# Kernel optimization log

Hardware: AMD Instinct MI355X
Metric: run time of the kernel (lower is better)

The kernel has to match this reference:

```python
import jax, jax.numpy as jnp
import numpy as np

TRAN_DIM = 768
N_HEADS = 8
HEAD_DIM = 96
INNER = N_HEADS * HEAD_DIM  # 768


def setup_inputs() -> dict:
    key = jax.random.key(0)
    k1, k2, k3, k4, k5 = jax.random.split(key, 5)
    x = jax.random.normal(k1, (16, 1024, TRAN_DIM), dtype=jnp.float32)
    s_in = 1.0 / np.sqrt(TRAN_DIM)
    W_qkv = jax.random.uniform(k2, (TRAN_DIM, INNER * 3), jnp.float32, -s_in, s_in)
    b_qkv = jax.random.uniform(k3, (INNER * 3,), jnp.float32, -s_in, s_in)
    s_o = 1.0 / np.sqrt(INNER)
    W_out = jax.random.uniform(k4, (INNER, TRAN_DIM), jnp.float32, -s_o, s_o)
    b_out = jax.random.uniform(k5, (TRAN_DIM,), jnp.float32, -s_o, s_o)
    return {"x": x, "W_qkv": W_qkv, "b_qkv": b_qkv, "W_out": W_out, "b_out": b_out}


def reference(x, W_qkv, b_qkv, W_out, b_out):
    B, N, _ = x.shape
    qkv = x @ W_qkv + b_qkv  # [B, N, 3*INNER]
    q, k, v = jnp.split(qkv, 3, axis=-1)
    # [B, N, INNER] -> [B, H, N, D]
    def to_heads(t):
        return t.reshape(B, N, N_HEADS, HEAD_DIM).transpose(0, 2, 1, 3)
    q, k, v = to_heads(q), to_heads(k), to_heads(v)
    scale = HEAD_DIM ** (-0.5)
    dots = jnp.einsum('bhnd,bhmd->bhnm', q, k) * scale
    attn = jax.nn.softmax(dots, axis=-1)
    out = jnp.einsum('bhnm,bhmd->bhnd', attn, v)
    out = out.transpose(0, 2, 1, 3).reshape(B, N, INNER)
    return out @ W_out + b_out
```

## Files before the change

### kernel.cpp

```cpp
#include <hip/hip_runtime.h>
#include <hip/hip_bf16.h>


#define DEVINL __device__ __forceinline__

typedef __attribute__((ext_vector_type(8))) short s16x8;
typedef __attribute__((ext_vector_type(4))) short s16x4;
typedef __attribute__((ext_vector_type(4))) float f32x4;
typedef __attribute__((ext_vector_type(16))) float f32x16;

DEVINL short f2bf(float f) {
  union { float f; unsigned u; } c; c.f = f;
  unsigned r = c.u + 0x7FFFu + ((c.u >> 16) & 1u);
  return (short)(r >> 16);
}
DEVINL float asf(unsigned u) {
  union { unsigned u; float f; } c; c.u = u; return c.f;
}
DEVINL unsigned pack2(float a, float b) {
  union { float f; unsigned u; } ca, cb; ca.f = a; cb.f = b;
  return (ca.u >> 16) | (cb.u & 0xffff0000u);
}
DEVINL int swap23(int k) { return (k & ~12) | ((k & 4) << 1) | ((k & 8) >> 1); }

DEVINL void gload_lds16(const short* g, short* lds) {
  __builtin_amdgcn_global_load_lds((const __attribute__((address_space(1))) void*)g,
                                   (__attribute__((address_space(3))) void*)lds, 16, 0, 0);
}


__global__ void cvt_x_kernel(const float* __restrict__ in, short* __restrict__ out) {
  int i = blockIdx.x * 256 + threadIdx.x;
  float4 v = ((const float4*)in)[i];
  s16x4 o = { f2bf(v.x), f2bf(v.y), f2bf(v.z), f2bf(v.w) };
  *(s16x4*)(out + (size_t)i * 4) = o;
}

__global__ void tcvt_kernel(const float* __restrict__ in, short* __restrict__ out, int R, int C) {
  __shared__ float t[32][33];
  int tx = threadIdx.x & 31, ty = threadIdx.x >> 5;
  int r0 = blockIdx.y * 32, c0 = blockIdx.x * 32;
#pragma unroll
  for (int i = 0; i < 4; i++) {
    int r = ty + i * 8;
    t[r][tx] = in[(size_t)(r0 + r) * C + c0 + tx];
  }
  __syncthreads();
#pragma unroll
  for (int i = 0; i < 4; i++) {
    int r = ty + i * 8;
    out[(size_t)(c0 + r) * R + r0 + tx] = f2bf(t[tx][r]);
  }
}

__global__ void vtrans_kernel(const short* __restrict__ qkvb, short* __restrict__ out) {
  __shared__ short t[32][34];
  int tx = threadIdx.x & 31, ty = threadIdx.x >> 5;
  int d0 = blockIdx.x * 32, n0 = blockIdx.y * 32;
  int pair = blockIdx.z;
  int b = pair >> 3, h = pair & 7;
#pragma unroll
  for (int i = 0; i < 4; i++) {
    int r = ty + i * 8;
    t[r][tx] = qkvb[(size_t)(b * 1024 + n0 + r) * 2304 + 1536 + h * 96 + d0 + tx];
  }
  __syncthreads();
  size_t obase = (size_t)pair * 96 * 1024;
#pragma unroll
  for (int i = 0; i < 4; i++) {
    int r = ty + i * 8;
    out[obase + (size_t)(d0 + r) * 1024 + n0 + tx] = t[tx][r];
  }
}


template <int MODE>
__global__ __launch_bounds__(512, 4) void gemm2(const short* __restrict__ A, const short* __restrict__ Bt,
                                                const float* __restrict__ bias, int K, int nTn,
                                                short* __restrict__ qkvb, float* __restrict__ outf) {
  __shared__ short lds[32768];
  short* const ldsA = lds;
  short* const ldsB = lds + 16384;
  const int tid = threadIdx.x;
  const int l = tid & 63, w = tid >> 6;
  const int lo = l & 15, hi = l >> 4;
  const int wm = w >> 1, wn = w & 1;

  int cpx = gridDim.x >> 3;
  int bid = blockIdx.x;
  int swz = (bid & 7) * cpx + (bid >> 3);
  int tm = swz / nTn, tn = swz - tm * nTn;

  const int NKT = K >> 5;

  const int Ls = tid >> 3, s7 = tid & 7;
  const int pS = (s7 >> 2) & 1;
  const int cS = (s7 & 3) ^ (Ls & 3);
  const int rho = 2 * Ls + pS;
  const int gA = ((rho >> 5) << 6) + (rho & 31);
  const short* aS0 = A + (size_t)(tm * 256 + gA) * K + cS * 8;
  const short* aS1 = aS0 + (size_t)32 * K;
  const short* bS = Bt + (size_t)(tn * 128 + rho) * K + cS * 8;
  short* const aD = ldsA + tid * 8;
  short* const bD = ldsB + tid * 8;

#define ST_A(j, q) gload_lds16(((q) ? aS1 : aS0) + (j) * 32, aD + (((j) & 1) * 2 + (q)) * 4096)
#define ST_B(j)    gload_lds16(bS + (j) * 32, bD + ((j) & 1) * 4096)

  const int LaBase = wm * 16 + (lo >> 1);
  const int LbBase = wn * 32 + (lo >> 1);
  const int pp = (lo & 1) << 2;

  f32x4 acc[4][4] = {};

#define RD_A(AF, buf, qm) do {                                                   \
    const short* base_ = ldsA + ((buf) * 2 + (qm)) * 4096;                       \
    _Pragma("unroll") for (int mi = 0; mi < 2; mi++) {                           \
      int La_ = LaBase + mi * 8;                                                 \
      AF[mi] = *(const s16x8*)(base_ + La_ * 64 + (((hi ^ (La_ & 3)) + pp) << 3)); } } while (0)
#define RD_B(BF, buf) do {                                                       \
    const short* base_ = ldsB + (buf) * 4096;                                    \
    _Pragma("unroll") for (int b = 0; b < 4; b++) {                              \
      int Lb_ = LbBase + b * 8;                                                  \
      BF[b] = *(const s16x8*)(base_ + Lb_ * 64 + (((hi ^ (Lb_ & 3)) + pp) << 3)); } } while (0)

#define MM8(a0, AF, BF) do {                                                     \
    __builtin_amdgcn_s_setprio(1);                                               \
    _Pragma("unroll") for (int mi = 0; mi < 2; mi++)                             \
      _Pragma("unroll") for (int b = 0; b < 4; b++)                              \
        acc[(a0) + mi][b] = __builtin_amdgcn_mfma_f32_16x16x32_bf16(             \
            AF[mi], BF[b], acc[(a0) + mi][b], 0, 0, 0);                          \
    __builtin_amdgcn_s_setprio(0);                                               \
    __builtin_amdgcn_sched_barrier(0); } while (0)

#define WAITV(n) asm volatile("s_waitcnt vmcnt(" #n ")" ::: "memory")
#define BARR() do { __builtin_amdgcn_sched_barrier(0); __builtin_amdgcn_s_barrier(); \
                    __builtin_amdgcn_sched_barrier(0); } while (0)

  ST_A(0, 0); ST_A(0, 1); ST_B(0);
  ST_A(1, 0); ST_B(1);
  WAITV(2);
  __builtin_amdgcn_s_barrier();

  s16x8 af[2], bf[4];
#pragma unroll 1
  for (int kt = 0; kt < NKT; kt++) {
    int buf = kt & 1;
    RD_A(af, buf, 0);
    RD_B(bf, buf);
    MM8(0, af, bf);
    if (kt + 1 < NKT) ST_A(kt + 1, 1);
    if (kt == NKT - 1) { WAITV(0); } else { WAITV(3); }
    BARR();
    RD_A(af, buf, 1);
    MM8(2, af, bf);
    if (kt + 2 < NKT) {
      ST_A(kt + 2, 0); ST_B(kt + 2);
      WAITV(3);
    } else {
      WAITV(0);
    }
    BARR();
  }
#undef ST_A
#undef ST_B
#undef RD_A
#undef RD_B
#undef MM8
#undef WAITV
#undef BARR

  if (MODE == 0) {
    const float qscale = 0.14724444757204526f;
    __syncthreads();
#pragma unroll
    for (int b = 0; b < 4; b++) {
      int colr = wn * 64 + b * 16 + lo;
      int coln = tn * 128 + colr;
      float bv = bias[coln];
      float scl = (coln < 768) ? qscale : 1.0f;
#pragma unroll
      for (int a = 0; a < 4; a++)
#pragma unroll
        for (int j = 0; j < 4; j++) {
          int rowr = wm * 64 + a * 16 + hi * 4 + j;
          lds[rowr * 128 + colr] = f2bf((acc[a][b][j] + bv) * scl);
        }
    }
    __syncthreads();
    short* dstb = qkvb + (size_t)(tm * 256) * 2304 + tn * 128;
#pragma unroll
    for (int k = 0; k < 8; k++) {
      int g = k * 512 + tid;
      int r = g >> 4, c = g & 15;
      *(s16x8*)(dstb + (size_t)r * 2304 + c * 8) = *(const s16x8*)(lds + r * 128 + c * 8);
    }
  } else {
#pragma unroll
    for (int b = 0; b < 4; b++) {
      int coln = tn * 128 + wn * 64 + b * 16 + lo;
      float bv = bias[coln];
#pragma unroll
      for (int a = 0; a < 4; a++)
#pragma unroll
        for (int j = 0; j < 4; j++) {
          int rowm = tm * 256 + wm * 64 + a * 16 + hi * 4 + j;
          outf[(size_t)rowm * 768 + coln] = acc[a][b][j] + bv;
        }
    }
  }
}


__global__ __launch_bounds__(256) void attn_kernel(const short* __restrict__ qkvb,
                                                   const short* __restrict__ vtb,
                                                   short* __restrict__ attn_out) {
  __shared__ short Klds[64 * 104];
  __shared__ short Vlds[96 * 64];
  int tid = threadIdx.x, lane = tid & 63, wid = tid >> 6;
  int q31 = lane & 31, hi2 = lane >> 5;
  int bid = blockIdx.x;
  int pair = bid & 127, qt = bid >> 7;
  int b = pair >> 3, h = pair & 7;
  const short* Vtp = vtb + (size_t)pair * 1024 * 96;
  int qrow0 = qt * 128 + wid * 32;

  s16x8 qf[6];
#pragma unroll
  for (int dc = 0; dc < 6; dc++)
    qf[dc] = *(const s16x8*)(qkvb + (size_t)(b * 1024 + qrow0 + q31) * 2304 +
                             h * 96 + dc * 16 + hi2 * 8);

  const short* sp[6];
  short* sdst[6];
  int sstep[6];
#pragma unroll
  for (int i = 0; i < 6; i++) {
    if (i < 3) {
      int c = i * 256 + tid;
      int krow = c / 12, kcc = c - krow * 12;
      int lam = swap23(krow);
      sdst[i] = Klds + lam * 104 + kcc * 8;
      sp[i] = qkvb + (size_t)(b * 1024 + krow) * 2304 + 768 + h * 96 + kcc * 8;
      sstep[i] = 64 * 2304;
    } else {
      int d = (i - 3) * 256 + tid;
      int vrow = d >> 3, vcc = d & 7;
      sdst[i] = Vlds + vrow * 64 + ((vcc ^ (vrow & 7)) << 3);
      sp[i] = Vtp + (size_t)vrow * 1024 + vcc * 8;
      sstep[i] = 64;
    }
  }

  f32x16 accO[3] = {};
  float lsum = 0.0f;

  s16x8 sreg[6];
#pragma unroll
  for (int i = 0; i < 6; i++) sreg[i] = *(const s16x8*)sp[i];

  for (int t = 0; t < 16; t++) {
    __syncthreads();
#pragma unroll
    for (int i = 0; i < 6; i++) *(s16x8*)sdst[i] = sreg[i];
    __syncthreads();

    int t2 = (t + 1) & 15;
#pragma unroll
    for (int i = 0; i < 6; i++)
      sreg[i] = *(const s16x8*)(sp[i] + (size_t)t2 * sstep[i]);

#pragma unroll
    for (int kb = 0; kb < 2; kb++) {
      f32x16 st = {};
#pragma unroll
      for (int dc = 0; dc < 6; dc++) {
        int c = dc * 2 + hi2;
        int lam = kb * 32 + q31;
        s16x8 kf = *(const s16x8*)(Klds + lam * 104 + c * 8);
        st = __builtin_amdgcn_mfma_f32_32x32x16_bf16(kf, qf[dc], st, 0, 0, 0);
      }

      unsigned u[8];
#pragma unroll
      for (int i = 0; i < 8; i++) {
        float p0 = __builtin_amdgcn_exp2f(st[2 * i]);
        float p1 = __builtin_amdgcn_exp2f(st[2 * i + 1]);
        unsigned w = pack2(p0, p1);
        u[i] = w;
        lsum += asf(w << 16) + asf(w & 0xffff0000u);
      }

#pragma unroll
      for (int half = 0; half < 2; half++) {
        union { unsigned w[4]; s16x8 v; } pa;
#pragma unroll
        for (int wi = 0; wi < 4; wi++) pa.w[wi] = u[half * 4 + wi];
        int kc = kb * 2 + half;
#pragma unroll
        for (int db = 0; db < 3; db++) {
          int d = db * 32 + q31;
          s16x8 vf = *(const s16x8*)(Vlds + d * 64 + (((kc * 2 + hi2) ^ (d & 7)) << 3));
          accO[db] = __builtin_amdgcn_mfma_f32_32x32x16_bf16(pa.v, vf, accO[db], 0, 0, 0);
        }
      }
    }
  }

  float s = lsum + __shfl_xor(lsum, 32, 64);
  float rinv = 1.0f / s;
  float rr[16];
#pragma unroll
  for (int r = 0; r < 16; r++)
    rr[r] = __shfl(rinv, (r & 3) + 8 * (r >> 2) + 4 * hi2, 64);

#pragma unroll
  for (int db = 0; db < 3; db++)
#pragma unroll
    for (int r = 0; r < 16; r++) {
      int qrow = qrow0 + (r & 3) + 8 * (r >> 2) + 4 * hi2;
      int d = db * 32 + q31;
      attn_out[((size_t)b * 1024 + qrow) * 768 + h * 96 + d] = f2bf(accO[db][r] * rr[r]);
    }
}


extern "C" void kernel_launch(void* const* d_in, const int* in_sizes, int n_in,
                              void* d_out, int out_size, void* d_ws, size_t ws_size,
                              hipStream_t stream) {
  const float* x = (const float*)d_in[0];
  const float* Wqkv = (const float*)d_in[1];
  const float* bqkv = (const float*)d_in[2];
  const float* Wout = (const float*)d_in[3];
  const float* bout = (const float*)d_in[4];
  float* out = (float*)d_out;

  char* ws = (char*)d_ws;
  short* xb = (short*)ws;
  short* wqkvT = (short*)(ws + 25165824);
  short* woutT = (short*)(ws + 28704768);
  short* qkvb = (short*)(ws + 29884416);
  short* vtb = (short*)(ws + 105381888);

  cvt_x_kernel<<<12288, 256, 0, stream>>>(x, xb);
  tcvt_kernel<<<dim3(72, 24), 256, 0, stream>>>(Wqkv, wqkvT, 768, 2304);
  tcvt_kernel<<<dim3(24, 24), 256, 0, stream>>>(Wout, woutT, 768, 768);

  gemm2<0><<<1152, 512, 0, stream>>>(xb, wqkvT, bqkv, 768, 18, qkvb, nullptr);
  vtrans_kernel<<<dim3(3, 32, 128), 256, 0, stream>>>(qkvb, vtb);
  attn_kernel<<<1024, 256, 0, stream>>>(qkvb, vtb, xb);
  gemm2<1><<<384, 512, 0, stream>>>(xb, woutT, bout, 768, 6, nullptr, out);
}
```

Before: 189.4 us.

## Triple-buffer LDS in GEMM mainloop to drop mid-iteration barrier

Grows the shared-memory staging from two to three buffers for the A and B tiles and rotates through them with a circular index. Loads for tile kt+2 are issued into the free buffer, so the mid-iteration wait and barrier go away and only one barrier per k-step remains. The aim is to cut synchronisation stalls and get more overlap between global-to-LDS loads and MFMA work. The cost is more LDS per block (72KB), which may lower how many blocks fit on each CU under launch_bounds(512,4).

Result: no change. 187.9 us (-0.8%).

```diff
diff --git a/kernel.cpp b/kernel.cpp
--- a/kernel.cpp
+++ b/kernel.cpp
@@ -78,9 +78,9 @@
 __global__ __launch_bounds__(512, 4) void gemm2(const short* __restrict__ A, const short* __restrict__ Bt,
                                                 const float* __restrict__ bias, int K, int nTn,
                                                 short* __restrict__ qkvb, float* __restrict__ outf) {
-  __shared__ short lds[32768];
+  __shared__ short lds[36864];
   short* const ldsA = lds;
-  short* const ldsB = lds + 16384;
+  short* const ldsB = lds + 24576;
   const int tid = threadIdx.x;
   const int l = tid & 63, w = tid >> 6;
   const int lo = l & 15, hi = l >> 4;
@@ -101,11 +101,9 @@
   const short* aS0 = A + (size_t)(tm * 256 + gA) * K + cS * 8;
   const short* aS1 = aS0 + (size_t)32 * K;
   const short* bS = Bt + (size_t)(tn * 128 + rho) * K + cS * 8;
-  short* const aD = ldsA + tid * 8;
-  short* const bD = ldsB + tid * 8;
-
-#define ST_A(j, q) gload_lds16(((q) ? aS1 : aS0) + (j) * 32, aD + (((j) & 1) * 2 + (q)) * 4096)
-#define ST_B(j)    gload_lds16(bS + (j) * 32, bD + ((j) & 1) * 4096)
+
+#define ST_A(j, q, bs) gload_lds16(((q) ? aS1 : aS0) + (j) * 32, ldsA + ((bs) * 2 + (q)) * 4096 + tid * 8)
+#define ST_B(j, bs)    gload_lds16(bS + (j) * 32, ldsB + (bs) * 4096 + tid * 8)
 
   const int LaBase = wm * 16 + (lo >> 1);
   const int LbBase = wn * 32 + (lo >> 1);
@@ -113,13 +111,13 @@
 
   f32x4 acc[4][4] = {};
 
-#define RD_A(AF, buf, qm) do {                                                   \
-    const short* base_ = ldsA + ((buf) * 2 + (qm)) * 4096;                       \
+#define RD_A(AF, bc, qm) do {                                                    \
+    const short* base_ = ldsA + ((bc) * 2 + (qm)) * 4096;                        \
     _Pragma("unroll") for (int mi = 0; mi < 2; mi++) {                           \
       int La_ = LaBase + mi * 8;                                                 \
       AF[mi] = *(const s16x8*)(base_ + La_ * 64 + (((hi ^ (La_ & 3)) + pp) << 3)); } } while (0)
-#define RD_B(BF, buf) do {                                                       \
-    const short* base_ = ldsB + (buf) * 4096;                                    \
+#define RD_B(BF, bc) do {                                                        \
+    const short* base_ = ldsB + (bc) * 4096;                                     \
     _Pragma("unroll") for (int b = 0; b < 4; b++) {                              \
       int Lb_ = LbBase + b * 8;                                                  \
       BF[b] = *(const s16x8*)(base_ + Lb_ * 64 + (((hi ^ (Lb_ & 3)) + pp) << 3)); } } while (0)
@@ -137,30 +135,30 @@
 #define BARR() do { __builtin_amdgcn_sched_barrier(0); __builtin_amdgcn_s_barrier(); \
                     __builtin_amdgcn_sched_barrier(0); } while (0)
 
-  ST_A(0, 0); ST_A(0, 1); ST_B(0);
-  ST_A(1, 0); ST_B(1);
-  WAITV(2);
+  ST_A(0, 0, 0); ST_B(0, 0); ST_A(0, 1, 0);
+  ST_A(1, 0, 1); ST_B(1, 1); ST_A(1, 1, 1);
+  WAITV(3);
   __builtin_amdgcn_s_barrier();
 
   s16x8 af[2], bf[4];
+  int bc = 0;
 #pragma unroll 1
   for (int kt = 0; kt < NKT; kt++) {
-    int buf = kt & 1;
-    RD_A(af, buf, 0);
-    RD_B(bf, buf);
+    int bs = (bc == 0) ? 2 : bc - 1;
+    RD_A(af, bc, 0);
+    RD_B(bf, bc);
     MM8(0, af, bf);
-    if (kt + 1 < NKT) ST_A(kt + 1, 1);
-    if (kt == NKT - 1) { WAITV(0); } else { WAITV(3); }
-    BARR();
-    RD_A(af, buf, 1);
+    if (kt + 2 < NKT) { ST_A(kt + 2, 0, bs); ST_B(kt + 2, bs); }
+    RD_A(af, bc, 1);
     MM8(2, af, bf);
     if (kt + 2 < NKT) {
-      ST_A(kt + 2, 0); ST_B(kt + 2);
+      ST_A(kt + 2, 1, bs);
       WAITV(3);
-    } else {
+    } else if (kt + 2 == NKT) {
       WAITV(0);
     }
     BARR();
+    bc = (bc == 2) ? 0 : bc + 1;
   }
 #undef ST_A
 #undef ST_B
```

## Fuse V transpose into QKV GEMM epilogue and shrink LDS for occupancy

Applied to the files above, without the earlier changes.

Removes the separate V-transpose kernel by having the QKV GEMM write V tiles directly in transposed layout through a per-wave swizzled LDS scratch. The Q/K epilogue is split into two half-tile passes so LDS can shrink from 64KB to 48KB, and launch bounds rise to 6 blocks per CU. It also drops a sched_barrier in the MFMA macro and adds priority raising around MFMA sections in attention. This saves a kernel launch and a full global round trip of V, at the cost of extra barriers and scattered 16-byte stores in the epilogue.

Measured after the change: 698.7 us. 269% more time.

```diff
diff --git a/kernel.cpp b/kernel.cpp
--- a/kernel.cpp
+++ b/kernel.cpp
@@ -53,32 +53,13 @@
   }
 }
 
-__global__ void vtrans_kernel(const short* __restrict__ qkvb, short* __restrict__ out) {
-  __shared__ short t[32][34];
-  int tx = threadIdx.x & 31, ty = threadIdx.x >> 5;
-  int d0 = blockIdx.x * 32, n0 = blockIdx.y * 32;
-  int pair = blockIdx.z;
-  int b = pair >> 3, h = pair & 7;
-#pragma unroll
-  for (int i = 0; i < 4; i++) {
-    int r = ty + i * 8;
-    t[r][tx] = qkvb[(size_t)(b * 1024 + n0 + r) * 2304 + 1536 + h * 96 + d0 + tx];
-  }
-  __syncthreads();
-  size_t obase = (size_t)pair * 96 * 1024;
-#pragma unroll
-  for (int i = 0; i < 4; i++) {
-    int r = ty + i * 8;
-    out[obase + (size_t)(d0 + r) * 1024 + n0 + tx] = t[tx][r];
-  }
-}
-
 
 template <int MODE>
-__global__ __launch_bounds__(512, 4) void gemm2(const short* __restrict__ A, const short* __restrict__ Bt,
+__global__ __launch_bounds__(512, 6) void gemm2(const short* __restrict__ A, const short* __restrict__ Bt,
                                                 const float* __restrict__ bias, int K, int nTn,
-                                                short* __restrict__ qkvb, float* __restrict__ outf) {
-  __shared__ short lds[32768];
+                                                short* __restrict__ qkvb, short* __restrict__ vtb,
+                                                float* __restrict__ outf) {
+  __shared__ short lds[24576];
   short* const ldsA = lds;
   short* const ldsB = lds + 16384;
   const int tid = threadIdx.x;
@@ -130,8 +111,7 @@
       _Pragma("unroll") for (int b = 0; b < 4; b++)                              \
         acc[(a0) + mi][b] = __builtin_amdgcn_mfma_f32_16x16x32_bf16(             \
             AF[mi], BF[b], acc[(a0) + mi][b], 0, 0, 0);                          \
-    __builtin_amdgcn_s_setprio(0);                                               \
-    __builtin_amdgcn_sched_barrier(0); } while (0)
+    __builtin_amdgcn_s_setprio(0); } while (0)
 
 #define WAITV(n) asm volatile("s_waitcnt vmcnt(" #n ")" ::: "memory")
 #define BARR() do { __builtin_amdgcn_sched_barrier(0); __builtin_amdgcn_s_barrier(); \
@@ -173,27 +153,71 @@
   if (MODE == 0) {
     const float qscale = 0.14724444757204526f;
     __syncthreads();
-#pragma unroll
-    for (int b = 0; b < 4; b++) {
-      int colr = wn * 64 + b * 16 + lo;
-      int coln = tn * 128 + colr;
-      float bv = bias[coln];
-      float scl = (coln < 768) ? qscale : 1.0f;
-#pragma unroll
-      for (int a = 0; a < 4; a++)
-#pragma unroll
-        for (int j = 0; j < 4; j++) {
-          int rowr = wm * 64 + a * 16 + hi * 4 + j;
-          lds[rowr * 128 + colr] = f2bf((acc[a][b][j] + bv) * scl);
-        }
-    }
-    __syncthreads();
-    short* dstb = qkvb + (size_t)(tm * 256) * 2304 + tn * 128;
-#pragma unroll
-    for (int k = 0; k < 8; k++) {
-      int g = k * 512 + tid;
-      int r = g >> 4, c = g & 15;
-      *(s16x8*)(dstb + (size_t)r * 2304 + c * 8) = *(const s16x8*)(lds + r * 128 + c * 8);
+    if (tn < 12) {
+#pragma unroll
+      for (int hh2 = 0; hh2 < 2; hh2++) {
+        if ((wm >> 1) == hh2) {
+#pragma unroll
+          for (int b = 0; b < 4; b++) {
+            int colr = wn * 64 + b * 16 + lo;
+            int coln = tn * 128 + colr;
+            float bv = bias[coln];
+            float scl = (coln < 768) ? qscale : 1.0f;
+#pragma unroll
+            for (int a = 0; a < 4; a++)
+#pragma unroll
+              for (int j = 0; j < 4; j++) {
+                int rowr = (wm & 1) * 64 + a * 16 + hi * 4 + j;
+                lds[rowr * 128 + colr] = f2bf((acc[a][b][j] + bv) * scl);
+              }
+          }
+        }
+        __syncthreads();
+        short* dstb = qkvb + (size_t)(tm * 256 + hh2 * 128) * 2304 + tn * 128;
+#pragma unroll
+        for (int k = 0; k < 4; k++) {
+          int g = k * 512 + tid;
+          int r = g >> 4, c = g & 15;
+          *(s16x8*)(dstb + (size_t)r * 2304 + c * 8) = *(const s16x8*)(lds + r * 128 + c * 8);
+        }
+        __syncthreads();
+      }
+    } else {
+      short* scr = lds + w * 2048;
+      int r8 = l >> 3, k8 = l & 7;
+      int n0 = k8 * 8;
+      int rowg = tm * 256 + wm * 64;
+      int bb = rowg >> 10;
+      int nb = (rowg & 1023) + n0;
+#pragma unroll
+      for (int hb = 0; hb < 2; hb++) {
+#pragma unroll
+        for (int b2 = 0; b2 < 2; b2++) {
+          int b = hb * 2 + b2;
+          int c32 = b2 * 16 + lo;
+          float bv = bias[tn * 128 + wn * 64 + hb * 32 + c32];
+#pragma unroll
+          for (int a = 0; a < 4; a++)
+#pragma unroll
+            for (int j = 0; j < 4; j++) {
+              int row = a * 16 + hi * 4 + j;
+              int cs = (c32 >> 3) ^ ((row >> 3) & 3);
+              scr[row * 32 + cs * 8 + (c32 & 7)] = f2bf(acc[a][b][j] + bv);
+            }
+        }
+#pragma unroll
+        for (int p = 0; p < 4; p++) {
+          int c32 = p * 8 + r8;
+          int inner = tn * 128 + wn * 64 + hb * 32 + c32 - 1536;
+          int hh = inner / 96;
+          int dd = inner - hh * 96;
+          union { short v[8]; s16x8 x; } t;
+#pragma unroll
+          for (int j = 0; j < 8; j++)
+            t.v[j] = scr[(n0 + j) * 32 + ((p ^ (k8 & 3)) * 8) + r8];
+          *(s16x8*)(vtb + ((size_t)(bb * 8 + hh) * 96 + dd) * 1024 + nb) = t.x;
+        }
+      }
     }
   } else {
 #pragma unroll
@@ -273,6 +297,7 @@
 #pragma unroll
     for (int kb = 0; kb < 2; kb++) {
       f32x16 st = {};
+      __builtin_amdgcn_s_setprio(1);
 #pragma unroll
       for (int dc = 0; dc < 6; dc++) {
         int c = dc * 2 + hi2;
@@ -280,6 +305,7 @@
         s16x8 kf = *(const s16x8*)(Klds + lam * 104 + c * 8);
         st = __builtin_amdgcn_mfma_f32_32x32x16_bf16(kf, qf[dc], st, 0, 0, 0);
       }
+      __builtin_amdgcn_s_setprio(0);
 
       unsigned u[8];
 #pragma unroll
@@ -291,6 +317,7 @@
         lsum += asf(w << 16) + asf(w & 0xffff0000u);
       }
 
+      __builtin_amdgcn_s_setprio(1);
 #pragma unroll
       for (int half = 0; half < 2; half++) {
         union { unsigned w[4]; s16x8 v; } pa;
@@ -304,6 +331,7 @@
           accO[db] = __builtin_amdgcn_mfma_f32_32x32x16_bf16(pa.v, vf, accO[db], 0, 0, 0);
         }
       }
+      __builtin_amdgcn_s_setprio(0);
     }
   }
 
@@ -346,8 +374,7 @@
   tcvt_kernel<<<dim3(72, 24), 256, 0, stream>>>(Wqkv, wqkvT, 768, 2304);
   tcvt_kernel<<<dim3(24, 24), 256, 0, stream>>>(Wout, woutT, 768, 768);
 
-  gemm2<0><<<1152, 512, 0, stream>>>(xb, wqkvT, bqkv, 768, 18, qkvb, nullptr);
-  vtrans_kernel<<<dim3(3, 32, 128), 256, 0, stream>>>(qkvb, vtb);
+  gemm2<0><<<1152, 512, 0, stream>>>(xb, wqkvT, bqkv, 768, 18, qkvb, vtb, nullptr);
   attn_kernel<<<1024, 256, 0, stream>>>(qkvb, vtb, xb);
-  gemm2<1><<<384, 512, 0, stream>>>(xb, woutT, bout, 768, 6, nullptr, out);
-}
+  gemm2<1><<<384, 512, 0, stream>>>(xb, woutT, bout, 768, 6, nullptr, nullptr, out);
+}
```
